# Kernel optimization log

Measured on AMD Instinct MI355X. Metric: run time of the kernel, lower is better.

Reference implementation:

```python
import jax, jax.numpy as jnp
import numpy as np

B, S, D, H, DH = 4, 2048, 1024, 16, 64  # batch, seq, d_model, heads, head_dim


def setup_inputs() -> dict:
    key = jax.random.key(0)
    ks = jax.random.split(key, 5)
    sc_in = 1.0 / np.sqrt(D)
    return {
        "x": jax.random.normal(ks[0], (B, S, D), dtype=jnp.float32),
        "Wq": jax.random.normal(ks[1], (H, D, DH), dtype=jnp.float32) * sc_in,
        "Wk": jax.random.normal(ks[2], (H, D, DH), dtype=jnp.float32) * sc_in,
        "Wv": jax.random.normal(ks[3], (H, D, DH), dtype=jnp.float32) * sc_in,
        "Wo": jax.random.normal(ks[4], (D, D), dtype=jnp.float32) * sc_in,
        "bo": jnp.zeros((D,), dtype=jnp.float32),
    }


def reference(x, Wq, Wk, Wv, Wo, bo):
    # Per-head Q/K/V projections (all heads batched in one einsum each).
    q = jnp.einsum("bsd,hde->bhse", x, Wq)  # [B,H,S,DH]
    k = jnp.einsum("bsd,hde->bhse", x, Wk)
    v = jnp.einsum("bsd,hde->bhse", x, Wv)
    scale = 1.0 / jnp.sqrt(jnp.asarray(DH, dtype=x.dtype))
    scores = jnp.einsum("bhse,bhte->bhst", q, k) * scale  # [B,H,S,S]
    causal = jnp.tril(jnp.ones((S, S), dtype=bool))
    scores = jnp.where(causal, scores, jnp.asarray(-jnp.inf, dtype=scores.dtype))
    attn = jax.nn.softmax(scores, axis=-1)
    heads = jnp.einsum("bhst,bhte->bhse", attn, v)  # [B,H,S,DH]
    # Concat heads (head-major order matches torch.cat of per-head outputs).
    concat = heads.transpose(0, 2, 1, 3).reshape(B, S, D)
    out = jnp.einsum("bsd,df->bsf", concat, Wo) + bo
    return out  # dropout_rate = 0.0 -> identity
```

## Files before the change

kernel.cpp:

```cpp
#include <hip/hip_runtime.h>
#include <hip/hip_bf16.h>

typedef __attribute__((ext_vector_type(8))) short short8;
typedef __attribute__((ext_vector_type(4))) short short4x;
typedef __attribute__((ext_vector_type(4))) float floatx4;
typedef __attribute__((ext_vector_type(16))) float floatx16;
typedef __attribute__((ext_vector_type(4))) unsigned uintx4;

__device__ __forceinline__ short f2bf(float f) {
    unsigned u = __float_as_uint(f);
    u = u + 0x7fffu + ((u >> 16) & 1u);
    return (short)(u >> 16);
}
__device__ __forceinline__ short f2bf_rz(float f) {
    return (short)(__float_as_uint(f) >> 16);
}

static constexpr int B_ = 4, S_ = 2048, D_ = 1024, H_ = 16, DH_ = 64;
static constexpr float QSCALE = 0.125f * 1.4426950408889634f;

__global__ __launch_bounds__(256) void convert_x(const float* __restrict__ in,
                                                 short* __restrict__ out, int n8) {
    int i = blockIdx.x * 256 + threadIdx.x;
    if (i >= n8) return;
    const float4* p = (const float4*)(in + (size_t)i * 8);
    float4 a = p[0], b = p[1];
    short8 v;
    v[0] = f2bf(a.x); v[1] = f2bf(a.y); v[2] = f2bf(a.z); v[3] = f2bf(a.w);
    v[4] = f2bf(b.x); v[5] = f2bf(b.y); v[6] = f2bf(b.z); v[7] = f2bf(b.w);
    *(short8*)(out + (size_t)i * 8) = v;
}

__global__ __launch_bounds__(256) void prep_weights(const float* __restrict__ Wq,
                                                    const float* __restrict__ Wk,
                                                    const float* __restrict__ Wv,
                                                    const float* __restrict__ Wo,
                                                    short* __restrict__ WqT,
                                                    short* __restrict__ WkT,
                                                    short* __restrict__ WvT,
                                                    short* __restrict__ WoT) {
    __shared__ alignas(16) float t[64 * 68];
    int z = blockIdx.z;
    const float* in;
    short* out;
    int N, M = D_, n0;
    if (z < 3) {
        const float* I = (z == 0) ? Wq : (z == 1) ? Wk : Wv;
        short* O = (z == 0) ? WqT : (z == 1) ? WkT : WvT;
        in = I + (size_t)blockIdx.y * D_ * DH_;
        out = O + (size_t)blockIdx.y * D_ * DH_;
        N = DH_; n0 = 0;
    } else {
        in = Wo; out = WoT; N = D_; n0 = blockIdx.y * 64;
    }
    int m0 = blockIdx.x * 64;
    int tid = threadIdx.x;
#pragma unroll
    for (int i = 0; i < 4; ++i) {
        int c = tid + i * 256;
        int row = c >> 4, c4 = (c & 15) * 4;
        float4 v = *(const float4*)(in + (size_t)(m0 + row) * N + n0 + c4);
        *(float4*)(t + row * 68 + c4) = v;
    }
    __syncthreads();
#pragma unroll
    for (int i = 0; i < 2; ++i) {
        int c = tid + i * 256;
        int row = c >> 3, c8 = (c & 7) * 8;
        short8 v;
#pragma unroll
        for (int j = 0; j < 8; ++j) v[j] = f2bf(t[(c8 + j) * 68 + row]);
        *(short8*)(out + (size_t)(n0 + row) * M + m0 + c8) = v;
    }
}

__device__ __forceinline__ void gemm128_core(const short* __restrict__ A,
                                             const short* __restrict__ Bm,
                                             short* ldsA, short* ldsB,
                                             int m0, int n0,
                                             floatx4 (&acc)[4][4],
                                             int w, int lane, int quad, int lm) {
    const int K = 1024;
    int wm = (w >> 1) * 64, wn = (w & 1) * 64;
    int rsub = lane >> 3;
    int csw = ((lane & 7) ^ rsub) * 8;
    int lmx = lm & 7;
    for (int k0 = 0; k0 < K; k0 += 64) {
#pragma unroll
        for (int i = 0; i < 4; ++i) {
            int r0 = w * 32 + i * 8;
            const short* ga = A + (size_t)(m0 + r0 + rsub) * K + k0 + csw;
            __builtin_amdgcn_global_load_lds((const __attribute__((address_space(1))) void*)ga,
                                             (__attribute__((address_space(3))) void*)(ldsA + r0 * 64),
                                             16, 0, 0);
            const short* gb = Bm + (size_t)(n0 + r0 + rsub) * K + k0 + csw;
            __builtin_amdgcn_global_load_lds((const __attribute__((address_space(1))) void*)gb,
                                             (__attribute__((address_space(3))) void*)(ldsB + r0 * 64),
                                             16, 0, 0);
        }
        __syncthreads();
#pragma unroll
        for (int ks = 0; ks < 2; ++ks) {
            short8 am[4], bn[4];
#pragma unroll
            for (int i = 0; i < 4; ++i)
                am[i] = *(const short8*)(ldsA + (wm + i * 16 + lm) * 64 + (((ks * 4 + quad) ^ lmx) << 3));
#pragma unroll
            for (int i = 0; i < 4; ++i)
                bn[i] = *(const short8*)(ldsB + (wn + i * 16 + lm) * 64 + (((ks * 4 + quad) ^ lmx) << 3));
#pragma unroll
            for (int mi = 0; mi < 4; ++mi)
#pragma unroll
                for (int ni = 0; ni < 4; ++ni)
                    acc[mi][ni] = __builtin_amdgcn_mfma_f32_16x16x32_bf16(am[mi], bn[ni], acc[mi][ni], 0, 0, 0);
        }
        __syncthreads();
    }
}

__global__ __launch_bounds__(256, 3) void qkv_gemm128(const short* __restrict__ xb,
                                                      const short* __restrict__ WqT,
                                                      const short* __restrict__ WkT,
                                                      const short* __restrict__ WvT,
                                                      short* __restrict__ Q,
                                                      short* __restrict__ K,
                                                      short* __restrict__ VT) {
    __shared__ alignas(16) short lds[16384];
    short* ldsA = lds;
    short* ldsB = lds + 8192;
    int m0 = blockIdx.x * 128, n0 = blockIdx.y * 128, z = blockIdx.z;
    const short* Bm = (z == 0) ? WqT : (z == 1) ? WkT : WvT;
    int tid = threadIdx.x, w = tid >> 6, lane = tid & 63, quad = lane >> 4, lm = lane & 15;

    floatx4 acc[4][4];
#pragma unroll
    for (int mi = 0; mi < 4; ++mi)
#pragma unroll
        for (int ni = 0; ni < 4; ++ni) acc[mi][ni] = (floatx4)0.0f;

    gemm128_core(xb, Bm, ldsA, ldsB, m0, n0, acc, w, lane, quad, lm);

    int wm = (w >> 1) * 64, wn = (w & 1) * 64;
    int b = m0 >> 11;
    int sbase = m0 & 2047;

    if (z < 2) {
        short* O = (z == 0) ? Q : K;
        float scale = (z == 0) ? QSCALE : 1.0f;
        short* t = lds;
#pragma unroll
        for (int ph = 0; ph < 2; ++ph) {
            if (ph) __syncthreads();
            if ((w & 1) == ph) {
#pragma unroll
                for (int mi = 0; mi < 4; ++mi)
#pragma unroll
                    for (int ni = 0; ni < 4; ++ni)
#pragma unroll
                        for (int r = 0; r < 4; ++r)
                            t[(wm + mi * 16 + quad * 4 + r) * 68 + ni * 16 + lm] =
                                f2bf(acc[mi][ni][r] * scale);
            }
            __syncthreads();
            int h = (n0 + ph * 64) >> 6;
            size_t obase = ((size_t)(b * 16 + h) * 2048 + sbase) * 64;
#pragma unroll
            for (int i = 0; i < 4; ++i) {
                int c = tid + i * 256;
                int m = c >> 3, e8 = (c & 7) * 8;
                short8 v = *(const short8*)(t + m * 68 + e8);
                *(short8*)(O + obase + (size_t)m * 64 + e8) = v;
            }
        }
    } else {
        short* t = lds;
#pragma unroll
        for (int ph = 0; ph < 2; ++ph) {
            if (ph) __syncthreads();
            if ((w & 1) == ph) {
#pragma unroll
                for (int mi = 0; mi < 4; ++mi)
#pragma unroll
                    for (int ni = 0; ni < 4; ++ni) {
                        int nl = ni * 16 + lm;
#pragma unroll
                        for (int r = 0; r < 4; ++r) {
                            int ml = wm + mi * 16 + quad * 4 + r;
                            t[nl * 136 + ml] = f2bf(acc[mi][ni][r]);
                        }
                    }
            }
            __syncthreads();
#pragma unroll
            for (int i = 0; i < 4; ++i) {
                int c = tid + i * 256;
                int rowl = c >> 4, colc = (c & 15) * 8;
                short8 v = *(const short8*)(t + rowl * 136 + colc);
                size_t n = n0 + ph * 64 + rowl;
                *(short8*)(VT + ((size_t)b * 1024 + n) * 2048 + sbase + colc) = v;
            }
        }
    }
}

__global__ __launch_bounds__(256, 3) void outproj128(const short* __restrict__ CC,
                                                     const short* __restrict__ WoT,
                                                     const float* __restrict__ bo,
                                                     float* __restrict__ out) {
    __shared__ alignas(16) short lds[16384];
    short* ldsA = lds;
    short* ldsB = lds + 8192;
    int m0 = blockIdx.x * 128, n0 = blockIdx.y * 128;
    int tid = threadIdx.x, w = tid >> 6, lane = tid & 63, quad = lane >> 4, lm = lane & 15;

    floatx4 acc[4][4];
#pragma unroll
    for (int mi = 0; mi < 4; ++mi)
#pragma unroll
        for (int ni = 0; ni < 4; ++ni) acc[mi][ni] = (floatx4)0.0f;

    gemm128_core(CC, WoT, ldsA, ldsB, m0, n0, acc, w, lane, quad, lm);

    int wm = (w >> 1) * 64, wn = (w & 1) * 64;
#pragma unroll
    for (int mi = 0; mi < 4; ++mi)
#pragma unroll
        for (int ni = 0; ni < 4; ++ni) {
            int n = n0 + wn + ni * 16 + lm;
            float bb = bo[n];
#pragma unroll
            for (int r = 0; r < 4; ++r) {
                int m = m0 + wm + mi * 16 + quad * 4 + r;
                out[(size_t)m * 1024 + n] = acc[mi][ni][r] + bb;
            }
        }
}

__global__ __launch_bounds__(256, 2) void attn_kernel(const short* __restrict__ Q,
                                                      const short* __restrict__ Kb,
                                                      const short* __restrict__ VT,
                                                      short* __restrict__ CC) {
    __shared__ alignas(16) short Kt[128 * 64];
    __shared__ alignas(16) short Vt[64 * 128];
    int bh = blockIdx.x;
    int pi = blockIdx.y;
    int b = bh >> 4, h = bh & 15;
    int tid = threadIdx.x;
    int w = tid >> 6, l = tid & 63;
    int hi = l >> 5, l31 = l & 31, l7 = l & 7;
    int rsub = l >> 3;
    int csw = ((l & 7) ^ rsub) * 8;
    int vr4 = l >> 4;
    int vc = l & 15;

    const short* Qbh = Q + (size_t)bh * S_ * DH_;
    const short* Kbh = Kb + (size_t)bh * S_ * DH_;
    const short* Vbh = VT + (size_t)bh * 64 * S_;

    for (int ps = 0; ps < 2; ++ps) {
        int qt = ps ? (15 - pi) : pi;
        int q0 = qt * 128;
        int qrow = q0 + w * 32 + l31;

        short8 qa[4];
        const short* Qrow = Qbh + (size_t)qrow * DH_;
#pragma unroll
        for (int ks = 0; ks < 4; ++ks)
            qa[ks] = *(const short8*)(Qrow + ks * 16 + hi * 8);

        floatx16 acc[2];
        acc[0] = (floatx16)0.0f;
        acc[1] = (floatx16)0.0f;
        float lsum = 0.0f;

        int nkt = qt + 1;
        for (int kt = 0; kt < nkt; ++kt) {
            int t0 = kt * 128;
            const short* Ktile = Kbh + (size_t)t0 * DH_;
#pragma unroll
            for (int i = 0; i < 4; ++i) {
                int r0 = w * 32 + i * 8;
                const short* ga = Ktile + (size_t)(r0 + rsub) * 64 + csw;
                __builtin_amdgcn_global_load_lds((const __attribute__((address_space(1))) void*)ga,
                                                 (__attribute__((address_space(3))) void*)(Kt + r0 * 64),
                                                 16, 0, 0);
            }
#pragma unroll
            for (int i = 0; i < 4; ++i) {
                int r0v = w * 16 + i * 4;
                int row = r0v + vr4;
                const short* gv = Vbh + (size_t)row * S_ + t0 + ((vc ^ (row & 7)) * 8);
                __builtin_amdgcn_global_load_lds((const __attribute__((address_space(1))) void*)gv,
                                                 (__attribute__((address_space(3))) void*)(Vt + r0v * 128),
                                                 16, 0, 0);
            }
            __syncthreads();

            floatx16 st[4];
            __builtin_amdgcn_s_setprio(1);
#pragma unroll
            for (int tb = 0; tb < 4; ++tb) {
                floatx16 t = (floatx16)0.0f;
#pragma unroll
                for (int ks = 0; ks < 4; ++ks) {
                    short8 kf = *(const short8*)(Kt + (tb * 32 + l31) * 64 +
                                                 (((ks * 2 + hi) ^ l7) << 3));
                    t = __builtin_amdgcn_mfma_f32_32x32x16_bf16(kf, qa[ks], t, 0, 0, 0);
                }
                st[tb] = t;
            }
            __builtin_amdgcn_s_setprio(0);

            if (kt == nkt - 1) {
#pragma unroll
                for (int tb = 0; tb < 4; ++tb)
#pragma unroll
                    for (int r = 0; r < 16; ++r) {
                        int t_ = t0 + tb * 32 + (r & 3) + 8 * (r >> 2) + 4 * hi;
                        if (t_ > qrow) st[tb][r] = -INFINITY;
                    }
            }

#pragma unroll
            for (int tb = 0; tb < 4; ++tb)
#pragma unroll
                for (int r = 0; r < 16; r += 4) {
                    float p0 = exp2f(st[tb][r]);
                    float p1 = exp2f(st[tb][r + 1]);
                    float p2 = exp2f(st[tb][r + 2]);
                    float p3 = exp2f(st[tb][r + 3]);
                    st[tb][r] = p0; st[tb][r + 1] = p1;
                    st[tb][r + 2] = p2; st[tb][r + 3] = p3;
                    lsum += (p0 + p1) + (p2 + p3);
                }

            __builtin_amdgcn_s_setprio(1);
#pragma unroll
            for (int tb = 0; tb < 4; ++tb)
#pragma unroll
                for (int sl = 0; sl < 2; ++sl) {
                    unsigned x0, y0, x1, y1;
                    asm("v_cvt_pk_bf16_f32 %0, %1, %2" : "=v"(x0)
                        : "v"(st[tb][sl * 8 + 0]), "v"(st[tb][sl * 8 + 1]));
                    asm("v_cvt_pk_bf16_f32 %0, %1, %2" : "=v"(y0)
                        : "v"(st[tb][sl * 8 + 4]), "v"(st[tb][sl * 8 + 5]));
                    asm("v_cvt_pk_bf16_f32 %0, %1, %2" : "=v"(x1)
                        : "v"(st[tb][sl * 8 + 2]), "v"(st[tb][sl * 8 + 3]));
                    asm("v_cvt_pk_bf16_f32 %0, %1, %2" : "=v"(y1)
                        : "v"(st[tb][sl * 8 + 6]), "v"(st[tb][sl * 8 + 7]));
                    asm("v_permlane32_swap_b32 %0, %1" : "+v"(x0), "+v"(y0));
                    asm("v_permlane32_swap_b32 %0, %1" : "+v"(x1), "+v"(y1));
                    uintx4 pd;
                    pd[0] = x0; pd[1] = x1; pd[2] = y0; pd[3] = y1;
                    short8 pa = __builtin_bit_cast(short8, pd);
                    int s = tb * 2 + sl;
#pragma unroll
                    for (int eb = 0; eb < 2; ++eb) {
                        short8 v = *(const short8*)(Vt + (eb * 32 + l31) * 128 +
                                                    (((s * 2 + hi) ^ l7) << 3));
                        acc[eb] = __builtin_amdgcn_mfma_f32_32x32x16_bf16(pa, v, acc[eb], 0, 0, 0);
                    }
                }
            __builtin_amdgcn_s_setprio(0);
            __syncthreads();
        }

        float lt = lsum + __shfl_xor(lsum, 32);
        float invl = 1.0f / lt;

#pragma unroll
        for (int r = 0; r < 16; ++r) {
            int q_local = (r & 3) + 8 * (r >> 2) + 4 * hi;
            float iv = __shfl(invl, q_local);
            int row = q0 + w * 32 + q_local;
            short* OC = CC + ((size_t)b * S_ + row) * D_ + h * DH_;
#pragma unroll
            for (int eb = 0; eb < 2; ++eb)
                OC[eb * 32 + l31] = f2bf(acc[eb][r] * iv);
        }
    }
}

extern "C" void kernel_launch(void* const* d_in, const int* in_sizes, int n_in,
                              void* d_out, int out_size, void* d_ws, size_t ws_size,
                              hipStream_t stream) {
    const float* x  = (const float*)d_in[0];
    const float* Wq = (const float*)d_in[1];
    const float* Wk = (const float*)d_in[2];
    const float* Wv = (const float*)d_in[3];
    const float* Wo = (const float*)d_in[4];
    const float* bo = (const float*)d_in[5];
    float* out = (float*)d_out;
    short* ws = (short*)d_ws;

    const size_t WSZ = (size_t)H_ * D_ * DH_;
    const size_t QSZ = (size_t)B_ * H_ * S_ * DH_;
    short* WqT = ws;
    short* WkT = WqT + WSZ;
    short* WvT = WkT + WSZ;
    short* WoT = WvT + WSZ;
    short* xb  = WoT + (size_t)D_ * D_;
    short* Qb  = xb + (size_t)B_ * S_ * D_;
    short* Kb  = Qb + QSZ;
    short* VTb = Kb + QSZ;
    short* CCb = VTb + QSZ;

    convert_x<<<(B_ * S_ * D_ / 8 + 255) / 256, 256, 0, stream>>>(x, xb, B_ * S_ * D_ / 8);
    prep_weights<<<dim3(16, 16, 4), 256, 0, stream>>>(Wq, Wk, Wv, Wo, WqT, WkT, WvT, WoT);
    qkv_gemm128<<<dim3(64, 8, 3), 256, 0, stream>>>(xb, WqT, WkT, WvT, Qb, Kb, VTb);
    attn_kernel<<<dim3(64, 8), 256, 0, stream>>>(Qb, Kb, VTb, CCb);
    outproj128<<<dim3(64, 8), 256, 0, stream>>>(CCb, WoT, bo, out);
}
```

Baseline: 235.6 us.

## Double-buffer K/V tiles in attention to prefetch next tile during compute

```diff
diff --git a/kernel.cpp b/kernel.cpp
--- a/kernel.cpp
+++ b/kernel.cpp
@@ -240,8 +240,8 @@
                                                       const short* __restrict__ Kb,
                                                       const short* __restrict__ VT,
                                                       short* __restrict__ CC) {
-    __shared__ alignas(16) short Kt[128 * 64];
-    __shared__ alignas(16) short Vt[64 * 128];
+    __shared__ alignas(16) short Kt[2 * 128 * 64];
+    __shared__ alignas(16) short Vt[2 * 64 * 128];
     int bh = blockIdx.x;
     int pi = blockIdx.y;
     int b = bh >> 4, h = bh & 15;
@@ -274,27 +274,53 @@
         float lsum = 0.0f;
 
         int nkt = qt + 1;
-        for (int kt = 0; kt < nkt; ++kt) {
-            int t0 = kt * 128;
-            const short* Ktile = Kbh + (size_t)t0 * DH_;
+
+        {
+            const short* Ktile = Kbh;
 #pragma unroll
             for (int i = 0; i < 4; ++i) {
                 int r0 = w * 32 + i * 8;
-                const short* ga = Ktile + (size_t)(r0 + rsub) * 64 + csw;
-                __builtin_amdgcn_global_load_lds((const __attribute__((address_space(1))) void*)ga,
-                                                 (__attribute__((address_space(3))) void*)(Kt + r0 * 64),
-                                                 16, 0, 0);
+                __builtin_amdgcn_global_load_lds(
+                    (const __attribute__((address_space(1))) void*)(Ktile + (size_t)(r0 + rsub) * 64 + csw),
+                    (__attribute__((address_space(3))) void*)(Kt + r0 * 64), 16, 0, 0);
             }
 #pragma unroll
             for (int i = 0; i < 4; ++i) {
                 int r0v = w * 16 + i * 4;
                 int row = r0v + vr4;
-                const short* gv = Vbh + (size_t)row * S_ + t0 + ((vc ^ (row & 7)) * 8);
-                __builtin_amdgcn_global_load_lds((const __attribute__((address_space(1))) void*)gv,
-                                                 (__attribute__((address_space(3))) void*)(Vt + r0v * 128),
-                                                 16, 0, 0);
-            }
-            __syncthreads();
+                __builtin_amdgcn_global_load_lds(
+                    (const __attribute__((address_space(1))) void*)(Vbh + (size_t)row * S_ + ((vc ^ (row & 7)) * 8)),
+                    (__attribute__((address_space(3))) void*)(Vt + r0v * 128), 16, 0, 0);
+            }
+        }
+        __syncthreads();
+
+        int cur = 0;
+        for (int kt = 0; kt < nkt; ++kt) {
+            int t0 = kt * 128;
+            if (kt + 1 < nkt) {
+                int t1 = t0 + 128;
+                int nx = cur ^ 1;
+                const short* Ktile = Kbh + (size_t)t1 * DH_;
+#pragma unroll
+                for (int i = 0; i < 4; ++i) {
+                    int r0 = w * 32 + i * 8;
+                    __builtin_amdgcn_global_load_lds(
+                        (const __attribute__((address_space(1))) void*)(Ktile + (size_t)(r0 + rsub) * 64 + csw),
+                        (__attribute__((address_space(3))) void*)(Kt + nx * 8192 + r0 * 64), 16, 0, 0);
+                }
+#pragma unroll
+                for (int i = 0; i < 4; ++i) {
+                    int r0v = w * 16 + i * 4;
+                    int row = r0v + vr4;
+                    __builtin_amdgcn_global_load_lds(
+                        (const __attribute__((address_space(1))) void*)(Vbh + (size_t)row * S_ + t1 + ((vc ^ (row & 7)) * 8)),
+                        (__attribute__((address_space(3))) void*)(Vt + nx * 8192 + r0v * 128), 16, 0, 0);
+                }
+            }
+
+            const short* Kc = Kt + cur * 8192;
+            const short* Vc = Vt + cur * 8192;
 
             floatx16 st[4];
             __builtin_amdgcn_s_setprio(1);
@@ -303,7 +329,7 @@
                 floatx16 t = (floatx16)0.0f;
 #pragma unroll
                 for (int ks = 0; ks < 4; ++ks) {
-                    short8 kf = *(const short8*)(Kt + (tb * 32 + l31) * 64 +
+                    short8 kf = *(const short8*)(Kc + (tb * 32 + l31) * 64 +
                                                  (((ks * 2 + hi) ^ l7) << 3));
                     t = __builtin_amdgcn_mfma_f32_32x32x16_bf16(kf, qa[ks], t, 0, 0, 0);
                 }
@@ -356,13 +382,14 @@
                     int s = tb * 2 + sl;
 #pragma unroll
                     for (int eb = 0; eb < 2; ++eb) {
-                        short8 v = *(const short8*)(Vt + (eb * 32 + l31) * 128 +
+                        short8 v = *(const short8*)(Vc + (eb * 32 + l31) * 128 +
                                                     (((s * 2 + hi) ^ l7) << 3));
                         acc[eb] = __builtin_amdgcn_mfma_f32_32x32x16_bf16(pa, v, acc[eb], 0, 0, 0);
                     }
                 }
             __builtin_amdgcn_s_setprio(0);
             __syncthreads();
+            cur ^= 1;
         }
 
         float lt = lsum + __shfl_xor(lsum, 32);
```

After: 239.3 us. Within noise of the previous version (+1.6%).
